# Kernel optimization log

Measured on AMD Instinct MI355X. Metric: run time of the kernel, lower is better.

The kernel has to match this reference:

```python
import jax, jax.numpy as jnp
import numpy as np

D_MODEL = 768
N_HEAD = 12
BATCH = 2
SEQ = 2048
MASK_FILL = -100000.0


def setup_inputs() -> dict:
    key = jax.random.key(0)
    ks = jax.random.split(key, 10)
    s = 1.0 / np.sqrt(D_MODEL)
    inp = {
        "xEnc": jax.random.normal(ks[0], (BATCH, SEQ, D_MODEL), jnp.float32),
        "xDec": jax.random.normal(ks[1], (BATCH, SEQ, D_MODEL), jnp.float32),
        # causal mask: True where attention is disallowed (j > i)
        "mask": (jnp.arange(SEQ)[None, :] > jnp.arange(SEQ)[:, None])[None, None, :, :],
        "wQ": jax.random.uniform(ks[2], (D_MODEL, D_MODEL), jnp.float32, -s, s),
        "bQ": jax.random.uniform(ks[3], (D_MODEL,), jnp.float32, -s, s),
        "wK": jax.random.uniform(ks[4], (D_MODEL, D_MODEL), jnp.float32, -s, s),
        "bK": jax.random.uniform(ks[5], (D_MODEL,), jnp.float32, -s, s),
        "wV": jax.random.uniform(ks[6], (D_MODEL, D_MODEL), jnp.float32, -s, s),
        "bV": jax.random.uniform(ks[7], (D_MODEL,), jnp.float32, -s, s),
        "wOut": jax.random.uniform(ks[8], (D_MODEL, D_MODEL), jnp.float32, -s, s),
        "bOut": jax.random.uniform(ks[9], (D_MODEL,), jnp.float32, -s, s),
    }
    return inp


def reference(xEnc, xDec, mask, wQ, bQ, wK, bK, wV, bV, wOut, bOut):
    B, S, D = xEnc.shape
    H = N_HEAD
    Dh = D // H
    # torch Linear: y = x @ W.T + b
    Q = xDec @ wQ.T + bQ
    K = xEnc @ wK.T + bK
    V = xEnc @ wV.T + bV
    Q = Q.reshape(B, S, H, Dh).transpose(0, 2, 1, 3)  # [B,H,S,Dh]
    K = K.reshape(B, S, H, Dh).transpose(0, 2, 1, 3)
    V = V.reshape(B, S, H, Dh).transpose(0, 2, 1, 3)
    score = jnp.einsum("bhqd,bhkd->bhqk", Q, K) / jnp.sqrt(jnp.float32(Dh))
    score = jnp.where(mask, MASK_FILL, score)
    attn = jax.nn.softmax(score, axis=-1)
    ctx = jnp.einsum("bhqk,bhkd->bhqd", attn, V)  # [B,H,S,Dh]
    ctx = ctx.transpose(0, 2, 1, 3).reshape(B, S, D)
    return ctx @ wOut.T + bOut
```

## Files before the change

### kernel.cpp

```cpp
#include <hip/hip_runtime.h>
#include <stdint.h>
#include <stddef.h>

#define DMODEL 768
#define NHEAD 12
#define SEQLEN 2048
#define NBATCH 2
#define DH 64
#define MTOT (NBATCH*SEQLEN)

typedef short s16x4 __attribute__((ext_vector_type(4)));
typedef short s16x8 __attribute__((ext_vector_type(8)));
typedef float f32x4 __attribute__((ext_vector_type(4)));

#define XDECB_OFF 0u
#define XENCB_OFF 3145728u
#define WQB_OFF   6291456u
#define WKB_OFF   6881280u
#define WVB_OFF   7471104u
#define WOUTB_OFF 8060928u
#define QB_OFF    8650752u
#define KB_OFF    11796480u
#define VT_OFF    14942208u
#define CTXB_OFF  18087936u

#define QSCALE 0.18033688011112042f

static __device__ __forceinline__ unsigned short f2bf(float f) {
  union { float f; unsigned int u; } v; v.f = f;
  unsigned int r = v.u + 0x7fffu + ((v.u >> 16) & 1u);
  return (unsigned short)(r >> 16);
}

static __device__ __forceinline__ unsigned int pack2bf(float f0, float f1) {
  union { float f; unsigned int u; } a, b; a.f = f0; b.f = f1;
  return __builtin_amdgcn_perm(b.u + 0x8000u, a.u + 0x8000u, 0x07060302u);
}

#if __has_builtin(__builtin_amdgcn_exp2f)
#define EXP2(x) __builtin_amdgcn_exp2f(x)
#else
#define EXP2(x) exp2f(x)
#endif

static __device__ __forceinline__ f32x4 mfma16(s16x4 a, s16x4 b, f32x4 c) {
  return __builtin_amdgcn_mfma_f32_16x16x16bf16_1k(a, b, c, 0, 0, 0);
}
static __device__ __forceinline__ f32x4 mfma32(s16x8 a, s16x8 b, f32x4 c) {
  return __builtin_amdgcn_mfma_f32_16x16x32_bf16(a, b, c, 0, 0, 0);
}

__global__ __launch_bounds__(256) void cvt_kernel(
    const float* __restrict__ xDec, const float* __restrict__ xEnc,
    const float* __restrict__ wQ, const float* __restrict__ wK,
    const float* __restrict__ wV, const float* __restrict__ wOut,
    unsigned short* __restrict__ ws)
{
  const int seg = blockIdx.y;
  const float* src;
  unsigned int n4, off;
  switch (seg) {
    case 0:  src = xDec; n4 = 786432; off = XDECB_OFF; break;
    case 1:  src = xEnc; n4 = 786432; off = XENCB_OFF; break;
    case 2:  src = wQ;   n4 = 147456; off = WQB_OFF;   break;
    case 3:  src = wK;   n4 = 147456; off = WKB_OFF;   break;
    case 4:  src = wV;   n4 = 147456; off = WVB_OFF;   break;
    default: src = wOut; n4 = 147456; off = WOUTB_OFF; break;
  }
  unsigned short* d = ws + off;
  const unsigned int stride = gridDim.x * blockDim.x;
  for (unsigned int i = blockIdx.x * blockDim.x + threadIdx.x; i < n4; i += stride) {
    const float4 v = ((const float4*)src)[i];
    s16x4 p;
    p[0] = (short)f2bf(v.x); p[1] = (short)f2bf(v.y);
    p[2] = (short)f2bf(v.z); p[3] = (short)f2bf(v.w);
    ((s16x4*)d)[i] = p;
  }
}

#define PSTR 40

__global__ __launch_bounds__(256, 3) void qkv_gemm(
    const unsigned short* __restrict__ xDecB, const unsigned short* __restrict__ xEncB,
    const unsigned short* __restrict__ wQB, const unsigned short* __restrict__ wKB,
    const unsigned short* __restrict__ wVB,
    const float* __restrict__ bQ, const float* __restrict__ bK, const float* __restrict__ bV,
    unsigned short* __restrict__ Qb, unsigned short* __restrict__ Kb,
    unsigned short* __restrict__ Vt)
{
  const int z = blockIdx.z;
  const unsigned short* __restrict__ A = (z == 0) ? xDecB : xEncB;
  const unsigned short* __restrict__ B = (z == 0) ? wQB : ((z == 1) ? wKB : wVB);
  const float* __restrict__ bias = (z == 0) ? bQ : ((z == 1) ? bK : bV);

  __shared__ unsigned short lA[128 * PSTR];
  __shared__ unsigned short lB[128 * PSTR];

  const int tid  = threadIdx.x;
  const int lane = tid & 63;
  const int wid  = tid >> 6;
  const int ln   = lane & 15;
  const int qd   = lane >> 4;
  const int m0 = blockIdx.x * 128;
  const int n0 = blockIdx.y * 128;
  const int wm = (wid & 1) * 64;
  const int wn = (wid >> 1) * 64;

  f32x4 acc[4][4] = {};
  s16x8 pA[2], pB[2];

  auto load_tile = [&](int k0) {
    #pragma unroll
    for (int i = 0; i < 2; ++i) {
      const int f = tid + i * 256;
      pA[i] = *(const s16x8*)(A + (size_t)(m0 + (f >> 2)) * DMODEL + k0 + (f & 3) * 8);
      pB[i] = *(const s16x8*)(B + (size_t)(n0 + (f >> 2)) * DMODEL + k0 + (f & 3) * 8);
    }
  };

  load_tile(0);
  for (int k0 = 0; k0 < DMODEL; k0 += 32) {
    #pragma unroll
    for (int i = 0; i < 2; ++i) {
      const int f = tid + i * 256;
      *(s16x8*)&lA[(f >> 2) * PSTR + (f & 3) * 8] = pA[i];
      *(s16x8*)&lB[(f >> 2) * PSTR + (f & 3) * 8] = pB[i];
    }
    __syncthreads();
    if (k0 + 32 < DMODEL) load_tile(k0 + 32);
    s16x8 af[4], bfr[4];
    #pragma unroll
    for (int i = 0; i < 4; ++i)
      af[i] = *(const s16x8*)&lA[(wm + i * 16 + ln) * PSTR + qd * 8];
    #pragma unroll
    for (int j = 0; j < 4; ++j)
      bfr[j] = *(const s16x8*)&lB[(wn + j * 16 + ln) * PSTR + qd * 8];
    #pragma unroll
    for (int i = 0; i < 4; ++i)
      #pragma unroll
      for (int j = 0; j < 4; ++j)
        acc[i][j] = mfma32(af[i], bfr[j], acc[i][j]);
    __syncthreads();
  }

  #pragma unroll
  for (int j = 0; j < 4; ++j) {
    const int n_g = n0 + wn + j * 16 + ln;
    const float bv = bias[n_g];
    const int h    = n_g >> 6;
    const int dcol = n_g & 63;
    #pragma unroll
    for (int i = 0; i < 4; ++i) {
      #pragma unroll
      for (int r = 0; r < 4; ++r) {
        const int m_g  = m0 + wm + i * 16 + qd * 4 + r;
        const int bb   = m_g >> 11;
        const int srow = m_g & 2047;
        const float val = acc[i][j][r] + bv;
        if (z == 0)
          Qb[((size_t)((bb * NHEAD + h) * SEQLEN + srow)) * DH + dcol] = f2bf(val * QSCALE);
        else if (z == 1)
          Kb[((size_t)((bb * NHEAD + h) * SEQLEN + srow)) * DH + dcol] = f2bf(val);
        else
          Vt[((size_t)((bb * NHEAD + h) * DH + dcol)) * SEQLEN + srow] = f2bf(val);
      }
    }
  }
}

__global__ __launch_bounds__(256, 3) void out_gemm(
    const unsigned short* __restrict__ ctx, const unsigned short* __restrict__ wOutB,
    const float* __restrict__ bOut, float* __restrict__ out)
{
  __shared__ unsigned short lA[128 * PSTR];
  __shared__ unsigned short lB[128 * PSTR];

  const int tid  = threadIdx.x;
  const int lane = tid & 63;
  const int wid  = tid >> 6;
  const int ln   = lane & 15;
  const int qd   = lane >> 4;
  const int m0 = blockIdx.x * 128;
  const int n0 = blockIdx.y * 128;
  const int wm = (wid & 1) * 64;
  const int wn = (wid >> 1) * 64;

  f32x4 acc[4][4] = {};
  s16x8 pA[2], pB[2];

  auto load_tile = [&](int k0) {
    #pragma unroll
    for (int i = 0; i < 2; ++i) {
      const int f = tid + i * 256;
      pA[i] = *(const s16x8*)(ctx + (size_t)(m0 + (f >> 2)) * DMODEL + k0 + (f & 3) * 8);
      pB[i] = *(const s16x8*)(wOutB + (size_t)(n0 + (f >> 2)) * DMODEL + k0 + (f & 3) * 8);
    }
  };

  load_tile(0);
  for (int k0 = 0; k0 < DMODEL; k0 += 32) {
    #pragma unroll
    for (int i = 0; i < 2; ++i) {
      const int f = tid + i * 256;
      *(s16x8*)&lA[(f >> 2) * PSTR + (f & 3) * 8] = pA[i];
      *(s16x8*)&lB[(f >> 2) * PSTR + (f & 3) * 8] = pB[i];
    }
    __syncthreads();
    if (k0 + 32 < DMODEL) load_tile(k0 + 32);
    s16x8 af[4], bfr[4];
    #pragma unroll
    for (int i = 0; i < 4; ++i)
      af[i] = *(const s16x8*)&lA[(wm + i * 16 + ln) * PSTR + qd * 8];
    #pragma unroll
    for (int j = 0; j < 4; ++j)
      bfr[j] = *(const s16x8*)&lB[(wn + j * 16 + ln) * PSTR + qd * 8];
    #pragma unroll
    for (int i = 0; i < 4; ++i)
      #pragma unroll
      for (int j = 0; j < 4; ++j)
        acc[i][j] = mfma32(af[i], bfr[j], acc[i][j]);
    __syncthreads();
  }

  #pragma unroll
  for (int j = 0; j < 4; ++j) {
    const int n_g = n0 + wn + j * 16 + ln;
    const float bv = bOut[n_g];
    #pragma unroll
    for (int i = 0; i < 4; ++i) {
      #pragma unroll
      for (int r = 0; r < 4; ++r) {
        const int m_g = m0 + wm + i * 16 + qd * 4 + r;
        out[(size_t)m_g * DMODEL + n_g] = acc[i][j][r] + bv;
      }
    }
  }
}

#define KVT 128
#define LKP 72
#define LVP 136

__global__ __launch_bounds__(256, 3) void attn_kernel(
    const unsigned short* __restrict__ Qb, const unsigned short* __restrict__ Kb,
    const unsigned short* __restrict__ Vt, unsigned short* __restrict__ ctx)
{
  __shared__ unsigned short lK[KVT * LKP];
  __shared__ unsigned short lV[DH * LVP];

  const int tid  = threadIdx.x;
  const int lane = tid & 63;
  const int wid  = tid >> 6;
  const int ln   = lane & 15;
  const int qd   = lane >> 4;
  const int bh = blockIdx.y;
  const int q0 = (gridDim.x - 1 - blockIdx.x) * 64;
  const int q_lane = q0 + wid * 16 + ln;

  s16x8 qf[2];
  {
    const unsigned short* Qrow = Qb + ((size_t)bh * SEQLEN + q_lane) * DH;
    qf[0] = *(const s16x8*)(Qrow + qd * 8);
    qf[1] = *(const s16x8*)(Qrow + 32 + qd * 8);
  }

  float m_run = -__builtin_inff();
  float l_run = 0.0f;
  f32x4 o_acc[4] = {};

  const unsigned short* Kbase = Kb + (size_t)bh * SEQLEN * DH;
  const unsigned short* Vbase = Vt + (size_t)bh * DH * SEQLEN;
  const int kv_end = q0 + 64;
  const int ntiles = (kv_end + KVT - 1) / KVT;

  s16x8 rK[4], rV[4];
  auto load_kv = [&](int kv0) {
    #pragma unroll
    for (int i = 0; i < 4; ++i) {
      const int f = tid + i * 256;
      rK[i] = *(const s16x8*)(Kbase + (size_t)(kv0 + (f >> 3)) * DH + (f & 7) * 8);
    }
    #pragma unroll
    for (int i = 0; i < 4; ++i) {
      const int f = tid + i * 256;
      rV[i] = *(const s16x8*)(Vbase + (size_t)(f >> 4) * SEQLEN + kv0 + (f & 15) * 8);
    }
  };

  load_kv(0);
  for (int t0 = 0; t0 < ntiles; ++t0) {
    const int kv0 = t0 * KVT;
    #pragma unroll
    for (int i = 0; i < 4; ++i) {
      const int f = tid + i * 256;
      *(s16x8*)&lK[(f >> 3) * LKP + (f & 7) * 8] = rK[i];
    }
    #pragma unroll
    for (int i = 0; i < 4; ++i) {
      const int f = tid + i * 256;
      *(s16x8*)&lV[(f >> 4) * LVP + (f & 15) * 8] = rV[i];
    }
    __syncthreads();
    if (t0 + 1 < ntiles) load_kv(kv0 + KVT);

    f32x4 s_acc[8] = {};
    #pragma unroll
    for (int kc = 0; kc < 2; ++kc) {
      #pragma unroll
      for (int t = 0; t < 8; ++t) {
        const s16x8 a = *(const s16x8*)&lK[(t * 16 + ln) * LKP + kc * 32 + qd * 8];
        s_acc[t] = mfma32(a, qf[kc], s_acc[t]);
      }
    }

    float tmax = -1e30f;
    if (kv0 + KVT > q0) {
      #pragma unroll
      for (int t = 0; t < 8; ++t) {
        #pragma unroll
        for (int r = 0; r < 4; ++r) {
          const int kv = kv0 + t * 16 + qd * 4 + r;
          float sv = s_acc[t][r];
          sv = (kv > q_lane) ? -1e30f : sv;
          s_acc[t][r] = sv;
          tmax = fmaxf(tmax, sv);
        }
      }
    } else {
      #pragma unroll
      for (int t = 0; t < 8; ++t) {
        #pragma unroll
        for (int r = 0; r < 4; ++r)
          tmax = fmaxf(tmax, s_acc[t][r]);
      }
    }
    tmax = fmaxf(tmax, __shfl_xor(tmax, 16));
    tmax = fmaxf(tmax, __shfl_xor(tmax, 32));
    const float m_new = fmaxf(m_run, tmax);
    const float alpha = EXP2(m_run - m_new);

    float rsum = 0.0f;
    s16x4 pf[8];
    #pragma unroll
    for (int t = 0; t < 8; ++t) {
      const float p0 = EXP2(s_acc[t][0] - m_new);
      const float p1 = EXP2(s_acc[t][1] - m_new);
      const float p2 = EXP2(s_acc[t][2] - m_new);
      const float p3 = EXP2(s_acc[t][3] - m_new);
      rsum += (p0 + p1) + (p2 + p3);
      union { unsigned int u[2]; s16x4 v; } pk;
      pk.u[0] = pack2bf(p0, p1);
      pk.u[1] = pack2bf(p2, p3);
      pf[t] = pk.v;
    }
    rsum += __shfl_xor(rsum, 16);
    rsum += __shfl_xor(rsum, 32);
    l_run = l_run * alpha + rsum;
    m_run = m_new;

    #pragma unroll
    for (int r = 0; r < 4; ++r) {
      const float ar = __shfl(alpha, qd * 4 + r);
      #pragma unroll
      for (int j = 0; j < 4; ++j) o_acc[j][r] *= ar;
    }

    #pragma unroll
    for (int t = 0; t < 8; ++t) {
      #pragma unroll
      for (int j = 0; j < 4; ++j) {
        const s16x4 b = *(const s16x4*)&lV[(j * 16 + ln) * LVP + t * 16 + qd * 4];
        o_acc[j] = mfma16(pf[t], b, o_acc[j]);
      }
    }
    __syncthreads();
  }

  const int bb = bh / NHEAD;
  const int h  = bh % NHEAD;
  #pragma unroll
  for (int r = 0; r < 4; ++r) {
    const float lr  = __shfl(l_run, qd * 4 + r);
    const float inv = 1.0f / lr;
    const int q_g = q0 + wid * 16 + qd * 4 + r;
    unsigned short* dst = ctx + ((size_t)bb * SEQLEN + q_g) * DMODEL + h * DH;
    #pragma unroll
    for (int j = 0; j < 4; ++j)
      dst[j * 16 + ln] = f2bf(o_acc[j][r] * inv);
  }
}

extern "C" void kernel_launch(void* const* d_in, const int* in_sizes, int n_in,
                              void* d_out, int out_size, void* d_ws, size_t ws_size,
                              hipStream_t stream)
{
  const float* xEnc = (const float*)d_in[0];
  const float* xDec = (const float*)d_in[1];
  const float* wQ   = (const float*)d_in[3];
  const float* bQ   = (const float*)d_in[4];
  const float* wK   = (const float*)d_in[5];
  const float* bK   = (const float*)d_in[6];
  const float* wV   = (const float*)d_in[7];
  const float* bV   = (const float*)d_in[8];
  const float* wOut = (const float*)d_in[9];
  const float* bOut = (const float*)d_in[10];

  unsigned short* ws = (unsigned short*)d_ws;

  cvt_kernel<<<dim3(512, 6), 256, 0, stream>>>(xDec, xEnc, wQ, wK, wV, wOut, ws);
  qkv_gemm<<<dim3(MTOT / 128, DMODEL / 128, 3), 256, 0, stream>>>(
      ws + XDECB_OFF, ws + XENCB_OFF, ws + WQB_OFF, ws + WKB_OFF, ws + WVB_OFF,
      bQ, bK, bV, ws + QB_OFF, ws + KB_OFF, ws + VT_OFF);
  attn_kernel<<<dim3(SEQLEN / 64, NBATCH * NHEAD), 256, 0, stream>>>(
      ws + QB_OFF, ws + KB_OFF, ws + VT_OFF, ws + CTXB_OFF);
  out_gemm<<<dim3(MTOT / 128, DMODEL / 128), 256, 0, stream>>>(
      ws + CTXB_OFF, ws + WOUTB_OFF, bOut, (float*)d_out);
}
```

Baseline: 204.6 us.

## Load GEMM tiles directly to LDS with swizzled layout and BK=64

Both projection GEMMs now move A/B tiles from global memory straight into LDS with global_load_lds 16-byte transfers, replacing register staging, and use an XOR-swizzled 64-wide K tile instead of a padded 32-wide one. This removes the register round trip and halves the number of barrier pairs per K loop, while the swizzle avoids LDS bank conflicts without padding. In exchange, the register prefetch overlap of the next tile with the MFMAs is gone (single buffer). LDS per block doubles, which may reduce occupancy.

```diff
diff --git a/kernel.cpp b/kernel.cpp
--- a/kernel.cpp
+++ b/kernel.cpp
@@ -48,6 +48,13 @@
 }
 static __device__ __forceinline__ f32x4 mfma32(s16x8 a, s16x8 b, f32x4 c) {
   return __builtin_amdgcn_mfma_f32_16x16x32_bf16(a, b, c, 0, 0, 0);
+}
+
+typedef __attribute__((address_space(3))) unsigned int lds_u32_t;
+typedef const __attribute__((address_space(1))) unsigned int glb_u32_t;
+static __device__ __forceinline__ void gl_lds16(const unsigned short* g,
+                                                unsigned short* l) {
+  __builtin_amdgcn_global_load_lds((glb_u32_t*)g, (lds_u32_t*)l, 16, 0, 0);
 }
 
 __global__ __launch_bounds__(256) void cvt_kernel(
@@ -78,7 +85,7 @@
   }
 }
 
-#define PSTR 40
+#define BK 64
 
 __global__ __launch_bounds__(256, 3) void qkv_gemm(
     const unsigned short* __restrict__ xDecB, const unsigned short* __restrict__ xEncB,
@@ -93,8 +100,8 @@
   const unsigned short* __restrict__ B = (z == 0) ? wQB : ((z == 1) ? wKB : wVB);
   const float* __restrict__ bias = (z == 0) ? bQ : ((z == 1) ? bK : bV);
 
-  __shared__ unsigned short lA[128 * PSTR];
-  __shared__ unsigned short lB[128 * PSTR];
+  __shared__ unsigned short lA[128 * BK];
+  __shared__ unsigned short lB[128 * BK];
 
   const int tid  = threadIdx.x;
   const int lane = tid & 63;
@@ -106,40 +113,43 @@
   const int wm = (wid & 1) * 64;
   const int wn = (wid >> 1) * 64;
 
+  int srow[4], scol[4];
+  #pragma unroll
+  for (int c = 0; c < 4; ++c) {
+    const int s = c * 256 + wid * 64 + lane;
+    srow[c] = s >> 3;
+    scol[c] = (((s & 7) ^ ((s >> 3) & 7)) * 8);
+  }
+
   f32x4 acc[4][4] = {};
-  s16x8 pA[2], pB[2];
-
-  auto load_tile = [&](int k0) {
-    #pragma unroll
-    for (int i = 0; i < 2; ++i) {
-      const int f = tid + i * 256;
-      pA[i] = *(const s16x8*)(A + (size_t)(m0 + (f >> 2)) * DMODEL + k0 + (f & 3) * 8);
-      pB[i] = *(const s16x8*)(B + (size_t)(n0 + (f >> 2)) * DMODEL + k0 + (f & 3) * 8);
-    }
-  };
-
-  load_tile(0);
-  for (int k0 = 0; k0 < DMODEL; k0 += 32) {
-    #pragma unroll
-    for (int i = 0; i < 2; ++i) {
-      const int f = tid + i * 256;
-      *(s16x8*)&lA[(f >> 2) * PSTR + (f & 3) * 8] = pA[i];
-      *(s16x8*)&lB[(f >> 2) * PSTR + (f & 3) * 8] = pB[i];
-    }
-    __syncthreads();
-    if (k0 + 32 < DMODEL) load_tile(k0 + 32);
-    s16x8 af[4], bfr[4];
-    #pragma unroll
-    for (int i = 0; i < 4; ++i)
-      af[i] = *(const s16x8*)&lA[(wm + i * 16 + ln) * PSTR + qd * 8];
-    #pragma unroll
-    for (int j = 0; j < 4; ++j)
-      bfr[j] = *(const s16x8*)&lB[(wn + j * 16 + ln) * PSTR + qd * 8];
-    #pragma unroll
-    for (int i = 0; i < 4; ++i)
-      #pragma unroll
-      for (int j = 0; j < 4; ++j)
-        acc[i][j] = mfma32(af[i], bfr[j], acc[i][j]);
+
+  for (int k0 = 0; k0 < DMODEL; k0 += BK) {
+    #pragma unroll
+    for (int c = 0; c < 4; ++c) {
+      const int ldsoff = (c * 256 + wid * 64) * 8;
+      gl_lds16(A + (size_t)(m0 + srow[c]) * DMODEL + k0 + scol[c], &lA[ldsoff]);
+      gl_lds16(B + (size_t)(n0 + srow[c]) * DMODEL + k0 + scol[c], &lB[ldsoff]);
+    }
+    __syncthreads();
+    #pragma unroll
+    for (int kc = 0; kc < 2; ++kc) {
+      s16x8 af[4], bfr[4];
+      #pragma unroll
+      for (int i = 0; i < 4; ++i) {
+        const int r = wm + i * 16 + ln;
+        af[i] = *(const s16x8*)&lA[r * 64 + (((kc * 4 + qd) ^ (r & 7)) * 8)];
+      }
+      #pragma unroll
+      for (int j = 0; j < 4; ++j) {
+        const int r = wn + j * 16 + ln;
+        bfr[j] = *(const s16x8*)&lB[r * 64 + (((kc * 4 + qd) ^ (r & 7)) * 8)];
+      }
+      #pragma unroll
+      for (int i = 0; i < 4; ++i)
+        #pragma unroll
+        for (int j = 0; j < 4; ++j)
+          acc[i][j] = mfma32(af[i], bfr[j], acc[i][j]);
+    }
     __syncthreads();
   }
 
@@ -155,14 +165,14 @@
       for (int r = 0; r < 4; ++r) {
         const int m_g  = m0 + wm + i * 16 + qd * 4 + r;
         const int bb   = m_g >> 11;
-        const int srow = m_g & 2047;
+        const int srow2 = m_g & 2047;
         const float val = acc[i][j][r] + bv;
         if (z == 0)
-          Qb[((size_t)((bb * NHEAD + h) * SEQLEN + srow)) * DH + dcol] = f2bf(val * QSCALE);
+          Qb[((size_t)((bb * NHEAD + h) * SEQLEN + srow2)) * DH + dcol] = f2bf(val * QSCALE);
         else if (z == 1)
-          Kb[((size_t)((bb * NHEAD + h) * SEQLEN + srow)) * DH + dcol] = f2bf(val);
+          Kb[((size_t)((bb * NHEAD + h) * SEQLEN + srow2)) * DH + dcol] = f2bf(val);
         else
-          Vt[((size_t)((bb * NHEAD + h) * DH + dcol)) * SEQLEN + srow] = f2bf(val);
+          Vt[((size_t)((bb * NHEAD + h) * DH + dcol)) * SEQLEN + srow2] = f2bf(val);
       }
     }
   }
@@ -172,8 +182,8 @@
     const unsigned short* __restrict__ ctx, const unsigned short* __restrict__ wOutB,
     const float* __restrict__ bOut, float* __restrict__ out)
 {
-  __shared__ unsigned short lA[128 * PSTR];
-  __shared__ unsigned short lB[128 * PSTR];
+  __shared__ unsigned short lA[128 * BK];
+  __shared__ unsigned short lB[128 * BK];
 
   const int tid  = threadIdx.x;
   const int lane = tid & 63;
@@ -185,40 +195,43 @@
   const int wm = (wid & 1) * 64;
   const int wn = (wid >> 1) * 64;
 
+  int srow[4], scol[4];
+  #pragma unroll
+  for (int c = 0; c < 4; ++c) {
+    const int s = c * 256 + wid * 64 + lane;
+    srow[c] = s >> 3;
+    scol[c] = (((s & 7) ^ ((s >> 3) & 7)) * 8);
+  }
+
   f32x4 acc[4][4] = {};
-  s16x8 pA[2], pB[2];
-
-  auto load_tile = [&](int k0) {
-    #pragma unroll
-    for (int i = 0; i < 2; ++i) {
-      const int f = tid + i * 256;
-      pA[i] = *(const s16x8*)(ctx + (size_t)(m0 + (f >> 2)) * DMODEL + k0 + (f & 3) * 8);
-      pB[i] = *(const s16x8*)(wOutB + (size_t)(n0 + (f >> 2)) * DMODEL + k0 + (f & 3) * 8);
-    }
-  };
-
-  load_tile(0);
-  for (int k0 = 0; k0 < DMODEL; k0 += 32) {
-    #pragma unroll
-    for (int i = 0; i < 2; ++i) {
-      const int f = tid + i * 256;
-      *(s16x8*)&lA[(f >> 2) * PSTR + (f & 3) * 8] = pA[i];
-      *(s16x8*)&lB[(f >> 2) * PSTR + (f & 3) * 8] = pB[i];
-    }
-    __syncthreads();
-    if (k0 + 32 < DMODEL) load_tile(k0 + 32);
-    s16x8 af[4], bfr[4];
-    #pragma unroll
-    for (int i = 0; i < 4; ++i)
-      af[i] = *(const s16x8*)&lA[(wm + i * 16 + ln) * PSTR + qd * 8];
-    #pragma unroll
-    for (int j = 0; j < 4; ++j)
-      bfr[j] = *(const s16x8*)&lB[(wn + j * 16 + ln) * PSTR + qd * 8];
-    #pragma unroll
-    for (int i = 0; i < 4; ++i)
-      #pragma unroll
-      for (int j = 0; j < 4; ++j)
-        acc[i][j] = mfma32(af[i], bfr[j], acc[i][j]);
+
+  for (int k0 = 0; k0 < DMODEL; k0 += BK) {
+    #pragma unroll
+    for (int c = 0; c < 4; ++c) {
+      const int ldsoff = (c * 256 + wid * 64) * 8;
+      gl_lds16(ctx + (size_t)(m0 + srow[c]) * DMODEL + k0 + scol[c], &lA[ldsoff]);
+      gl_lds16(wOutB + (size_t)(n0 + srow[c]) * DMODEL + k0 + scol[c], &lB[ldsoff]);
+    }
+    __syncthreads();
+    #pragma unroll
+    for (int kc = 0; kc < 2; ++kc) {
+      s16x8 af[4], bfr[4];
+      #pragma unroll
+      for (int i = 0; i < 4; ++i) {
+        const int r = wm + i * 16 + ln;
+        af[i] = *(const s16x8*)&lA[r * 64 + (((kc * 4 + qd) ^ (r & 7)) * 8)];
+      }
+      #pragma unroll
+      for (int j = 0; j < 4; ++j) {
+        const int r = wn + j * 16 + ln;
+        bfr[j] = *(const s16x8*)&lB[r * 64 + (((kc * 4 + qd) ^ (r & 7)) * 8)];
+      }
+      #pragma unroll
+      for (int i = 0; i < 4; ++i)
+        #pragma unroll
+        for (int j = 0; j < 4; ++j)
+          acc[i][j] = mfma32(af[i], bfr[j], acc[i][j]);
+    }
     __syncthreads();
   }
 
```

Measured after the change: 197.7 us. -3.4%, faster.
